# Kernel optimization log

Measured on AMD Instinct MI355X. Metric: run time of the kernel, lower is better.

## Reference

```python
import jax, jax.numpy as jnp
import numpy as np

IDIM = 192
NB_SAMPLES = 128
NB_RAYS = 16384


def setup_inputs() -> dict:
    key = jax.random.key(0)
    k1, k2, k3, k4 = jax.random.split(key, 4)
    # origins strictly inside the AABB [0, idim-1]^3 so every ray intersects
    x = jax.random.uniform(k1, (NB_RAYS, 3), dtype=jnp.float32) * (IDIM - 2.0) + 0.5
    d = jax.random.normal(k2, (NB_RAYS, 3), dtype=jnp.float32)
    # keep components away from 0 so 1/d is finite, then normalize
    d = jnp.where(jnp.abs(d) < 1e-3, 1e-3, d)
    d = d / jnp.linalg.norm(d, axis=1, keepdims=True)
    grid = jax.random.uniform(k3, (IDIM, IDIM, IDIM, 9), dtype=jnp.float32)
    opacity = jax.random.uniform(k4, (IDIM, IDIM, IDIM), dtype=jnp.float32)
    return {"x": x, "d": d, "grid": grid, "opacity": opacity}


def _intersect_ray_aabb(x, inv_d, idim):
    inf = jnp.float32(idim) ** 3
    box_min = jnp.zeros((1, 3), jnp.float32)
    box_max = jnp.full((1, 3), jnp.float32(idim - 1))
    t0 = (box_min - x) * inv_d
    t1 = (box_max - x) * inv_d
    tsmaller = jnp.minimum(t0, t1)
    tbigger = jnp.maximum(t0, t1)
    tmin = jnp.maximum(-inf, jnp.max(tsmaller, axis=1))
    tmax = jnp.minimum(inf, jnp.min(tbigger, axis=1))
    return tmin, tmax


def _forward(x, d, grid, opacity):
    idim = grid.shape[0]
    R = x.shape[0]
    inv_d = 1.0 / d
    tmin, tmax = _intersect_ray_aabb(x, inv_d, idim)
    # Uniform(tmin, tmax) samples, sorted per ray (torch .sample() is no-grad)
    u = jax.random.uniform(jax.random.key(1), (R, NB_SAMPLES), dtype=jnp.float32)
    samples = jnp.sort(tmin[:, None] + u * (tmax - tmin)[:, None], axis=1)
    samples = jax.lax.stop_gradient(samples)

    # sample points along rays: [R, S, 3]
    pts = x[:, None, :] + samples[..., None] * d[:, None, :]
    i0 = jnp.clip(jnp.floor(pts).astype(jnp.int32), 0, idim - 2)  # base corner
    frac = pts - i0.astype(pts.dtype)  # trilinear weights (delta_voxel = 1)
    fx, fy, fz = frac[..., 0], frac[..., 1], frac[..., 2]
    ix, iy, iz = i0[..., 0], i0[..., 1], i0[..., 2]

    harm = jnp.zeros(pts.shape[:2] + (9,), pts.dtype)  # [R, S, 9]
    opac = jnp.zeros(pts.shape[:2], pts.dtype)         # [R, S]
    for ox in (0, 1):
        wx = fx if ox else (1.0 - fx)
        for oy in (0, 1):
            wy = fy if oy else (1.0 - fy)
            for oz in (0, 1):
                wz = fz if oz else (1.0 - fz)
                w = wx * wy * wz
                gi, gj, gk = ix + ox, iy + oy, iz + oz
                harm = harm + w[..., None] * grid[gi, gj, gk]
                opac = opac + w * opacity[gi, gj, gk]

    # volumetric compositing over the first S-1 samples (vectorized form of
    # the original sequential transmittance loop)
    deltas = samples[:, 1:] - samples[:, :-1]            # [R, S-1]
    cur = deltas * opac[:, :-1]                          # per-step opacity
    cum_excl = jnp.concatenate(
        [jnp.zeros((R, 1), cur.dtype), jnp.cumsum(cur, axis=1)[:, :-1]], axis=1)
    trans = jnp.exp(-cum_excl)
    color_s = jax.nn.sigmoid(jnp.sum(harm[:, :-1, :], axis=-1))
    rays_color = jnp.sum(trans * (1.0 - jnp.exp(-cur)) * color_s, axis=1)
    return rays_color


def reference(x, d, grid, opacity):
    return _forward(x, d, grid, opacity)
```

## Files before the change

kernel.cpp:

```cpp
#include <hip/hip_runtime.h>
#include <hip/hip_fp16.h>
#include <cstdint>
#include <cstddef>

#define IDIM 192
#define NSAMP 128
#define NRAYS 16384
#define NVOX (IDIM * IDIM * IDIM)


__device__ __forceinline__ uint32_t rotl32(uint32_t x, int r) {
    return (x << r) | (x >> (32 - r));
}

__device__ __forceinline__ uint32_t threefry_bits(uint32_t i) {
    const uint32_t ks0 = 0u;
    const uint32_t ks1 = 1u;
    const uint32_t ks2 = 0x1BD11BDAu ^ ks0 ^ ks1;
    uint32_t x0 = 0u + ks0;
    uint32_t x1 = i + ks1;
#define TF_ROUND(r) { x0 += x1; x1 = rotl32(x1, (r)); x1 ^= x0; }
    TF_ROUND(13) TF_ROUND(15) TF_ROUND(26) TF_ROUND(6)
    x0 += ks1; x1 += ks2 + 1u;
    TF_ROUND(17) TF_ROUND(29) TF_ROUND(16) TF_ROUND(24)
    x0 += ks2; x1 += ks0 + 2u;
    TF_ROUND(13) TF_ROUND(15) TF_ROUND(26) TF_ROUND(6)
    x0 += ks0; x1 += ks1 + 3u;
    TF_ROUND(17) TF_ROUND(29) TF_ROUND(16) TF_ROUND(24)
    x0 += ks1; x1 += ks2 + 4u;
    TF_ROUND(13) TF_ROUND(15) TF_ROUND(26) TF_ROUND(6)
    x0 += ks2; x1 += ks0 + 5u;
#undef TF_ROUND
    return x0 ^ x1;
}

__global__ __launch_bounds__(256)
void fuse_kernel(const float* __restrict__ grid, const float* __restrict__ opacity,
                 __half2* __restrict__ tab) {
    __shared__ float sh[256 * 9];
    const int t = threadIdx.x;
    const int base = blockIdx.x * 256;
    const float* gp = grid + (size_t)base * 9;
    #pragma unroll
    for (int i = 0; i < 9; ++i) {
        sh[i * 256 + t] = gp[i * 256 + t];
    }
    __syncthreads();
    float s = 0.f;
    #pragma unroll
    for (int c = 0; c < 9; ++c) s += sh[t * 9 + c];
    const int v = base + t;
    const int xq = v / (IDIM * IDIM);
    const int rem = v - xq * (IDIM * IDIM);
    const int yq = rem / IDIM;
    const int zq = rem - yq * IDIM;
    const int idx = (xq >> 1) * 73728 + ((xq & 1) << 3)
                  + (yq >> 1) * 768   + ((yq & 1) << 2)
                  + (zq >> 2) * 16    + (zq & 3);
    tab[idx] = __floats2half2_rn(s, opacity[v]);
}

__global__ __launch_bounds__(128, 8)
void rf_kernel(const float* __restrict__ x, const float* __restrict__ d,
               const __half2* __restrict__ tab, float* __restrict__ out) {
    const int wave = threadIdx.x >> 6;
    const int lane = threadIdx.x & 63;
    const int r = blockIdx.x * 2 + wave;

    const float ox = x[r * 3 + 0], oy = x[r * 3 + 1], oz = x[r * 3 + 2];
    const float dx = d[r * 3 + 0], dy = d[r * 3 + 1], dz = d[r * 3 + 2];
    const float inv_dx = 1.f / dx, inv_dy = 1.f / dy, inv_dz = 1.f / dz;
    const float INF = 7077888.f;
    const float BMAX = (float)(IDIM - 1);

    float tmin = -INF, tmax = INF;
    {
        float t0 = (0.f - ox) * inv_dx, t1 = (BMAX - ox) * inv_dx;
        tmin = fmaxf(tmin, fminf(t0, t1)); tmax = fminf(tmax, fmaxf(t0, t1));
        t0 = (0.f - oy) * inv_dy; t1 = (BMAX - oy) * inv_dy;
        tmin = fmaxf(tmin, fminf(t0, t1)); tmax = fminf(tmax, fmaxf(t0, t1));
        t0 = (0.f - oz) * inv_dz; t1 = (BMAX - oz) * inv_dz;
        tmin = fmaxf(tmin, fminf(t0, t1)); tmax = fminf(tmax, fmaxf(t0, t1));
    }

    const uint32_t i0 = (uint32_t)(r * NSAMP + lane);
    const uint32_t b0 = threefry_bits(i0);
    const uint32_t b1 = threefry_bits(i0 + 64u);
    float u0 = __uint_as_float((b0 >> 9) | 0x3f800000u) - 1.0f;
    float u1 = __uint_as_float((b1 >> 9) | 0x3f800000u) - 1.0f;
    u0 = fmaxf(0.f, u0);
    u1 = fmaxf(0.f, u1);
    float v0 = tmin + u0 * (tmax - tmin);
    float v1 = tmin + u1 * (tmax - tmin);

#define BSTEP(J, K)                                                            \
    {                                                                          \
        const float p0 = __shfl_xor(v0, (J));                                  \
        const float p1 = __shfl_xor(v1, (J));                                  \
        const bool lower = (lane & (J)) == 0;                                  \
        const bool tm0 = (((lane) & (K)) == 0) == lower;                       \
        const bool tm1 = ((((lane) + 64) & (K)) == 0) == lower;                \
        v0 = tm0 ? fminf(v0, p0) : fmaxf(v0, p0);                              \
        v1 = tm1 ? fminf(v1, p1) : fmaxf(v1, p1);                              \
    }
    #pragma unroll
    for (int k = 2; k <= 64; k <<= 1) {
        #pragma unroll
        for (int j = k >> 1; j >= 1; j >>= 1) BSTEP(j, k)
    }
    {
        const float mn = fminf(v0, v1), mx = fmaxf(v0, v1);
        v0 = mn; v1 = mx;
    }
    #pragma unroll
    for (int j = 32; j >= 1; j >>= 1) BSTEP(j, 128)
#undef BSTEP

    const int odd = lane & 1;
    const int hs  = lane >> 1;
    float cumRay = 0.f, acc = 0.f;

    for (int k = 0; k < 4; ++k) {
        const int sk = k * 32 + hs;
        const bool valid = (sk < NSAMP - 1);

        float ts, tn;
        if (k < 2) {
            ts = __shfl(v0, sk);
            const float tnv = __shfl(v0, (sk + 1 > 63) ? 63 : sk + 1);
            const float s64 = __shfl(v1, 0);
            tn = (sk == 63) ? s64 : tnv;
        } else {
            ts = __shfl(v1, sk - 64);
            const int ti = sk - 63;
            tn = __shfl(v1, (ti > 63) ? 63 : ti);
        }

        const float px = ox + ts * dx;
        const float py = oy + ts * dy;
        const float pz = oz + ts * dz;
        int ix = (int)floorf(px); ix = ix < 0 ? 0 : (ix > IDIM - 2 ? IDIM - 2 : ix);
        int iy = (int)floorf(py); iy = iy < 0 ? 0 : (iy > IDIM - 2 ? IDIM - 2 : iy);
        int iz = (int)floorf(pz); iz = iz < 0 ? 0 : (iz > IDIM - 2 ? IDIM - 2 : iz);
        const float fx = px - (float)ix;
        const float fy = py - (float)iy;
        const float fz = pz - (float)iz;
        const float wxs = odd ? fx : (1.f - fx);
        const float wy0 = 1.f - fy, wy1 = fy;
        const float wz0 = 1.f - fz, wz1 = fz;
        const int xs = ix + odd;
        const int fs = (xs >> 1) * 73728 + ((xs & 1) << 3);
        const int g0 = (iy >> 1) * 768 + ((iy & 1) << 2);
        const int g1 = ((iy + 1) >> 1) * 768 + (((iy + 1) & 1) << 2);
        const int h0 = (iz >> 2) * 16 + (iz & 3);
        const int h1 = ((iz + 1) >> 2) * 16 + ((iz + 1) & 3);
        const float2 c00 = __half22float2(tab[fs + g0 + h0]);
        const float2 c01 = __half22float2(tab[fs + g0 + h1]);
        const float2 c10 = __half22float2(tab[fs + g1 + h0]);
        const float2 c11 = __half22float2(tab[fs + g1 + h1]);
        float hp = wxs * (wy0 * (wz0 * c00.x + wz1 * c01.x) +
                          wy1 * (wz0 * c10.x + wz1 * c11.x));
        float op = wxs * (wy0 * (wz0 * c00.y + wz1 * c01.y) +
                          wy1 * (wz0 * c10.y + wz1 * c11.y));
        const float hsv = hp + __shfl_xor(hp, 1);
        const float opv = op + __shfl_xor(op, 1);

        const float cur = (valid && !odd) ? (tn - ts) * opv : 0.f;
        float incl = cur;
        #pragma unroll
        for (int off = 1; off < 64; off <<= 1) {
            const float tmp = __shfl_up(incl, off);
            if (lane >= off) incl += tmp;
        }
        if (valid && !odd) {
            const float excl = cumRay + incl - cur;
            const float color = 1.f / (1.f + __expf(-hsv));
            acc += __expf(-excl) * (1.f - __expf(-cur)) * color;
        }
        cumRay += __shfl(incl, 63);
        if (cumRay >= 10.f) break;
    }

    #pragma unroll
    for (int off = 32; off > 0; off >>= 1) acc += __shfl_down(acc, off);
    if (lane == 0) out[r] = acc;
}

extern "C" void kernel_launch(void* const* d_in, const int* in_sizes, int n_in,
                              void* d_out, int out_size, void* d_ws, size_t ws_size,
                              hipStream_t stream) {
    const float* x       = (const float*)d_in[0];
    const float* d       = (const float*)d_in[1];
    const float* grid    = (const float*)d_in[2];
    const float* opacity = (const float*)d_in[3];
    float* out = (float*)d_out;

    fuse_kernel<<<NVOX / 256, 256, 0, stream>>>(grid, opacity, (__half2*)d_ws);
    rf_kernel<<<NRAYS / 2, 128, 0, stream>>>(x, d, (const __half2*)d_ws, out);
}
```

Measured before the change: 77.90 us.

## Move per-ray sample generation and sort into the grid prep kernel

Per-ray AABB intersection, threefry sampling and the bitonic sort now run in blocks of the first kernel, interleaved with the grid-fusion blocks every seventh block. The sorted samples go to workspace, and the render kernel just loads them. The aim is to hide the compute-bound sort inside the bandwidth-bound grid pass, at the cost of an extra 8 MB write and read of sorted samples.

```diff
diff --git a/kernel.cpp b/kernel.cpp
--- a/kernel.cpp
+++ b/kernel.cpp
@@ -7,6 +7,11 @@
 #define NSAMP 128
 #define NRAYS 16384
 #define NVOX (IDIM * IDIM * IDIM)
+#define NFUSE (NVOX / 256)
+#define NSORTB (NRAYS / 4)
+#define NBLK (NFUSE + NSORTB)
+#define SORT_PERIOD 7
+#define SORT_LIM (NSORTB * SORT_PERIOD)
 
 
 __device__ __forceinline__ uint32_t rotl32(uint32_t x, int r) {
@@ -35,86 +40,107 @@
 }
 
 __global__ __launch_bounds__(256)
-void fuse_kernel(const float* __restrict__ grid, const float* __restrict__ opacity,
-                 __half2* __restrict__ tab) {
-    __shared__ float sh[256 * 9];
-    const int t = threadIdx.x;
-    const int base = blockIdx.x * 256;
-    const float* gp = grid + (size_t)base * 9;
-    #pragma unroll
-    for (int i = 0; i < 9; ++i) {
-        sh[i * 256 + t] = gp[i * 256 + t];
+void prep_kernel(const float* __restrict__ grid, const float* __restrict__ opacity,
+                 const float* __restrict__ x, const float* __restrict__ dvec,
+                 __half2* __restrict__ tab, float* __restrict__ sts) {
+    const int b = blockIdx.x;
+    const bool is_sort = (b < SORT_LIM) && (b % SORT_PERIOD == 3);
+
+    if (is_sort) {
+        const int q = b / SORT_PERIOD;
+        const int wv = threadIdx.x >> 6;
+        const int lane = threadIdx.x & 63;
+        const int r = q * 4 + wv;
+
+        const float ox = x[r * 3 + 0], oy = x[r * 3 + 1], oz = x[r * 3 + 2];
+        const float dx = dvec[r * 3 + 0], dy = dvec[r * 3 + 1], dz = dvec[r * 3 + 2];
+        const float inv_dx = 1.f / dx, inv_dy = 1.f / dy, inv_dz = 1.f / dz;
+        const float INF = 7077888.f;
+        const float BMAX = (float)(IDIM - 1);
+
+        float tmin = -INF, tmax = INF;
+        {
+            float t0 = (0.f - ox) * inv_dx, t1 = (BMAX - ox) * inv_dx;
+            tmin = fmaxf(tmin, fminf(t0, t1)); tmax = fminf(tmax, fmaxf(t0, t1));
+            t0 = (0.f - oy) * inv_dy; t1 = (BMAX - oy) * inv_dy;
+            tmin = fmaxf(tmin, fminf(t0, t1)); tmax = fminf(tmax, fmaxf(t0, t1));
+            t0 = (0.f - oz) * inv_dz; t1 = (BMAX - oz) * inv_dz;
+            tmin = fmaxf(tmin, fminf(t0, t1)); tmax = fminf(tmax, fmaxf(t0, t1));
+        }
+
+        const uint32_t i0 = (uint32_t)(r * NSAMP + lane);
+        const uint32_t b0 = threefry_bits(i0);
+        const uint32_t b1 = threefry_bits(i0 + 64u);
+        float u0 = __uint_as_float((b0 >> 9) | 0x3f800000u) - 1.0f;
+        float u1 = __uint_as_float((b1 >> 9) | 0x3f800000u) - 1.0f;
+        u0 = fmaxf(0.f, u0);
+        u1 = fmaxf(0.f, u1);
+        float v0 = tmin + u0 * (tmax - tmin);
+        float v1 = tmin + u1 * (tmax - tmin);
+
+#define BSTEP(J, K)                                                            \
+        {                                                                      \
+            const float p0 = __shfl_xor(v0, (J));                              \
+            const float p1 = __shfl_xor(v1, (J));                              \
+            const bool lower = (lane & (J)) == 0;                              \
+            const bool tm0 = (((lane) & (K)) == 0) == lower;                   \
+            const bool tm1 = ((((lane) + 64) & (K)) == 0) == lower;            \
+            v0 = tm0 ? fminf(v0, p0) : fmaxf(v0, p0);                          \
+            v1 = tm1 ? fminf(v1, p1) : fmaxf(v1, p1);                          \
+        }
+        #pragma unroll
+        for (int k = 2; k <= 64; k <<= 1) {
+            #pragma unroll
+            for (int j = k >> 1; j >= 1; j >>= 1) BSTEP(j, k)
+        }
+        {
+            const float mn = fminf(v0, v1), mx = fmaxf(v0, v1);
+            v0 = mn; v1 = mx;
+        }
+        #pragma unroll
+        for (int j = 32; j >= 1; j >>= 1) BSTEP(j, 128)
+#undef BSTEP
+        sts[r * NSAMP + lane] = v0;
+        sts[r * NSAMP + 64 + lane] = v1;
+    } else {
+        __shared__ float sh[256 * 9];
+        const int t = threadIdx.x;
+        const int nsb = (b < SORT_LIM) ? (b + 3) / SORT_PERIOD : NSORTB;
+        const int base = (b - nsb) * 256;
+        const float* gp = grid + (size_t)base * 9;
+        #pragma unroll
+        for (int i = 0; i < 9; ++i) {
+            sh[i * 256 + t] = gp[i * 256 + t];
+        }
+        __syncthreads();
+        float s = 0.f;
+        #pragma unroll
+        for (int c = 0; c < 9; ++c) s += sh[t * 9 + c];
+        const int v = base + t;
+        const int xq = v / (IDIM * IDIM);
+        const int rem = v - xq * (IDIM * IDIM);
+        const int yq = rem / IDIM;
+        const int zq = rem - yq * IDIM;
+        const int idx = (xq >> 1) * 73728 + ((xq & 1) << 3)
+                      + (yq >> 1) * 768   + ((yq & 1) << 2)
+                      + (zq >> 2) * 16    + (zq & 3);
+        tab[idx] = __floats2half2_rn(s, opacity[v]);
     }
-    __syncthreads();
-    float s = 0.f;
-    #pragma unroll
-    for (int c = 0; c < 9; ++c) s += sh[t * 9 + c];
-    const int v = base + t;
-    const int xq = v / (IDIM * IDIM);
-    const int rem = v - xq * (IDIM * IDIM);
-    const int yq = rem / IDIM;
-    const int zq = rem - yq * IDIM;
-    const int idx = (xq >> 1) * 73728 + ((xq & 1) << 3)
-                  + (yq >> 1) * 768   + ((yq & 1) << 2)
-                  + (zq >> 2) * 16    + (zq & 3);
-    tab[idx] = __floats2half2_rn(s, opacity[v]);
 }
 
 __global__ __launch_bounds__(128, 8)
 void rf_kernel(const float* __restrict__ x, const float* __restrict__ d,
-               const __half2* __restrict__ tab, float* __restrict__ out) {
+               const __half2* __restrict__ tab, const float* __restrict__ sts,
+               float* __restrict__ out) {
     const int wave = threadIdx.x >> 6;
     const int lane = threadIdx.x & 63;
     const int r = blockIdx.x * 2 + wave;
 
     const float ox = x[r * 3 + 0], oy = x[r * 3 + 1], oz = x[r * 3 + 2];
     const float dx = d[r * 3 + 0], dy = d[r * 3 + 1], dz = d[r * 3 + 2];
-    const float inv_dx = 1.f / dx, inv_dy = 1.f / dy, inv_dz = 1.f / dz;
-    const float INF = 7077888.f;
-    const float BMAX = (float)(IDIM - 1);
-
-    float tmin = -INF, tmax = INF;
-    {
-        float t0 = (0.f - ox) * inv_dx, t1 = (BMAX - ox) * inv_dx;
-        tmin = fmaxf(tmin, fminf(t0, t1)); tmax = fminf(tmax, fmaxf(t0, t1));
-        t0 = (0.f - oy) * inv_dy; t1 = (BMAX - oy) * inv_dy;
-        tmin = fmaxf(tmin, fminf(t0, t1)); tmax = fminf(tmax, fmaxf(t0, t1));
-        t0 = (0.f - oz) * inv_dz; t1 = (BMAX - oz) * inv_dz;
-        tmin = fmaxf(tmin, fminf(t0, t1)); tmax = fminf(tmax, fmaxf(t0, t1));
-    }
-
-    const uint32_t i0 = (uint32_t)(r * NSAMP + lane);
-    const uint32_t b0 = threefry_bits(i0);
-    const uint32_t b1 = threefry_bits(i0 + 64u);
-    float u0 = __uint_as_float((b0 >> 9) | 0x3f800000u) - 1.0f;
-    float u1 = __uint_as_float((b1 >> 9) | 0x3f800000u) - 1.0f;
-    u0 = fmaxf(0.f, u0);
-    u1 = fmaxf(0.f, u1);
-    float v0 = tmin + u0 * (tmax - tmin);
-    float v1 = tmin + u1 * (tmax - tmin);
-
-#define BSTEP(J, K)                                                            \
-    {                                                                          \
-        const float p0 = __shfl_xor(v0, (J));                                  \
-        const float p1 = __shfl_xor(v1, (J));                                  \
-        const bool lower = (lane & (J)) == 0;                                  \
-        const bool tm0 = (((lane) & (K)) == 0) == lower;                       \
-        const bool tm1 = ((((lane) + 64) & (K)) == 0) == lower;                \
-        v0 = tm0 ? fminf(v0, p0) : fmaxf(v0, p0);                              \
-        v1 = tm1 ? fminf(v1, p1) : fmaxf(v1, p1);                              \
-    }
-    #pragma unroll
-    for (int k = 2; k <= 64; k <<= 1) {
-        #pragma unroll
-        for (int j = k >> 1; j >= 1; j >>= 1) BSTEP(j, k)
-    }
-    {
-        const float mn = fminf(v0, v1), mx = fmaxf(v0, v1);
-        v0 = mn; v1 = mx;
-    }
-    #pragma unroll
-    for (int j = 32; j >= 1; j >>= 1) BSTEP(j, 128)
-#undef BSTEP
+
+    const float v0 = sts[r * NSAMP + lane];
+    const float v1 = sts[r * NSAMP + 64 + lane];
 
     const int odd = lane & 1;
     const int hs  = lane >> 1;
@@ -195,6 +221,9 @@
     const float* opacity = (const float*)d_in[3];
     float* out = (float*)d_out;
 
-    fuse_kernel<<<NVOX / 256, 256, 0, stream>>>(grid, opacity, (__half2*)d_ws);
-    rf_kernel<<<NRAYS / 2, 128, 0, stream>>>(x, d, (const __half2*)d_ws, out);
-}
+    __half2* tab = (__half2*)d_ws;
+    float* sts = (float*)((char*)d_ws + (size_t)NVOX * sizeof(__half2));
+
+    prep_kernel<<<NBLK, 256, 0, stream>>>(grid, opacity, x, d, tab, sts);
+    rf_kernel<<<NRAYS / 2, 128, 0, stream>>>(x, d, tab, sts, out);
+}
```

After: 72.05 us (median of 2 runs). 1.08x faster.
